# Optimization experiments

Hardware: AMD Instinct MI355X
Metric: run time of the kernel (lower is better)

## Reference

```python
import jax, jax.numpy as jnp
import numpy as np

N = 100000   # nodes
E = 1600000  # edges
F = 256      # feature_dim
H = 64       # hidden_dim == out_channels
HEADS = 1


def setup_inputs() -> dict:
    key = jax.random.key(0)
    ks = jax.random.split(key, 12)
    x = jax.random.normal(ks[0], (N, F), dtype=jnp.float32)
    edge_index = jax.random.randint(ks[1], (2, E), 0, N, dtype=jnp.int32)
    s = 0.05
    params = {
        'W_proj': jax.random.normal(ks[2], (F, H), dtype=jnp.float32) * s,
        'b_proj': jnp.zeros((H,), dtype=jnp.float32),
        'Wq1': jax.random.normal(ks[3], (H, HEADS * H), dtype=jnp.float32) * s,
        'Wk1': jax.random.normal(ks[4], (H, HEADS * H), dtype=jnp.float32) * s,
        'Wv1': jax.random.normal(ks[5], (H, HEADS * H), dtype=jnp.float32) * s,
        'Wq2': jax.random.normal(ks[6], (H, HEADS * H), dtype=jnp.float32) * s,
        'Wk2': jax.random.normal(ks[7], (H, HEADS * H), dtype=jnp.float32) * s,
        'Wv2': jax.random.normal(ks[8], (H, HEADS * H), dtype=jnp.float32) * s,
        'W_sig': jax.random.normal(ks[9], (H, 1), dtype=jnp.float32) * s,
        'b_sig': jnp.zeros((1,), dtype=jnp.float32),
    }
    return {'x': x, 'edge_index': edge_index, **params}


def _gat_layer(x, src, dst, Wq, Wk, Wv):
    # x: [N, H]; src/dst: [E] (edge_index[0]=source j, edge_index[1]=dest i)
    n = x.shape[0]
    q = (x @ Wq).reshape(n, HEADS, H)
    k = (x @ Wk).reshape(n, HEADS, H)
    v = (x @ Wv).reshape(n, HEADS, H)
    # edge-wise scores: (q_i * k_j).sum(-1) / sqrt(out_channels)
    scores = jnp.einsum('ehc,ehc->eh', q[dst], k[src]) / np.float32(np.sqrt(H))
    alpha = jax.nn.relu(scores)                                  # [E, HEADS]
    # segment softmax over destination neighborhoods (numerically stable)
    m = jax.ops.segment_max(alpha, dst, num_segments=n)          # [N, HEADS]
    m = jnp.where(jnp.isfinite(m), m, jnp.float32(0.0))
    e = jnp.exp(alpha - m[dst])
    denom = jax.ops.segment_sum(e, dst, num_segments=n)
    a = e / (denom[dst] + jnp.float32(1e-16))                    # [E, HEADS]
    # scatter-weighted sum of values to destinations
    out = jax.ops.segment_sum(v[src] * a[:, :, None], dst, num_segments=n)
    return out.mean(axis=1), a                                   # [N, H], [E, HEADS]


def reference(x, edge_index, W_proj, b_proj, Wq1, Wk1, Wv1, Wq2, Wk2, Wv2, W_sig, b_sig):
    src, dst = edge_index[0], edge_index[1]
    h = jax.nn.gelu(x @ W_proj + b_proj, approximate=False)
    h, attn1 = _gat_layer(h, src, dst, Wq1, Wk1, Wv1)
    h = jax.nn.gelu(h, approximate=False)
    h, attn2 = _gat_layer(h, src, dst, Wq2, Wk2, Wv2)
    signals = h @ W_sig + b_sig                                  # [N, 1]
    return signals, attn1, attn2
```

## Files before the change

kernel.cpp:

```cpp
#include <hip/hip_runtime.h>
#include <hip/hip_fp16.h>
#include <math.h>

#define FF 256
#define HH 64

typedef __attribute__((ext_vector_type(8))) short short8;
typedef __attribute__((ext_vector_type(4))) float f32x4;

__device__ __forceinline__ float gelu_f(float x) {
    float ax = fabsf(x) * 0.70710678118654752f;
    float t = __builtin_amdgcn_rcpf(fmaf(0.3275911f, ax, 1.0f));
    float poly = t * fmaf(t, fmaf(t, fmaf(t, fmaf(t, 1.061405429f, -1.453152027f),
                  1.421413741f), -0.284496736f), 0.254829592f);
    float er = 1.0f - poly * __expf(-ax * ax);
    er = (x < 0.f) ? -er : er;
    return 0.5f * x * (1.0f + er);
}

__device__ __forceinline__ unsigned short bf16rne(float f) {
    unsigned u = __float_as_uint(f);
    unsigned r = u + 0x7FFFu + ((u >> 16) & 1u);
    return (unsigned short)(r >> 16);
}

__device__ __forceinline__ void bf16split(float f, short& hi, short& lo) {
    unsigned u = __float_as_uint(f);
    unsigned r = u + 0x7FFFu + ((u >> 16) & 1u);
    hi = (short)(r >> 16);
    float fh = __uint_as_float(r & 0xFFFF0000u);
    float fl = f - fh;
    unsigned u2 = __float_as_uint(fl);
    unsigned r2 = u2 + 0x7FFFu + ((u2 >> 16) & 1u);
    lo = (short)(r2 >> 16);
}

__device__ __forceinline__ __half2 shfl_xor_h2(__half2 v, int off) {
    union { __half2 h; int i; } u;
    u.h = v;
    u.i = __shfl_xor(u.i, off, 64);
    return u.h;
}

__global__ __launch_bounds__(256) void k_wprep(
        const float* __restrict__ Wp,
        const float* __restrict__ Wq1, const float* __restrict__ Wk1, const float* __restrict__ Wv1,
        const float* __restrict__ Wq2, const float* __restrict__ Wk2, const float* __restrict__ Wv2,
        short* __restrict__ wf) {
    int total = 16384 + 6 * 4096;
    for (int gid = blockIdx.x * 256 + threadIdx.x; gid < total; gid += gridDim.x * 256) {
        const float* W;
        int fid, hibase, lobase;
        if (gid < 16384) {
            W = Wp; fid = gid; hibase = 0; lobase = 16384;
        } else {
            int t = gid - 16384;
            int m = t >> 12;
            fid = t & 4095;
            switch (m) {
                case 0: W = Wq1; break;
                case 1: W = Wk1; break;
                case 2: W = Wv1; break;
                case 3: W = Wq2; break;
                case 4: W = Wk2; break;
                default: W = Wv2; break;
            }
            hibase = 32768 + m * 8192;
            lobase = hibase + 4096;
        }
        int j    = fid & 7;
        int lane = (fid >> 3) & 63;
        int ct   = (fid >> 9) & 3;
        int s    = fid >> 11;
        int k    = s * 32 + (lane >> 4) * 8 + j;
        int col  = ct * 16 + (lane & 15);
        short hi, lo;
        bf16split(W[k * HH + col], hi, lo);
        wf[hibase + fid] = hi;
        wf[lobase + fid] = lo;
    }
}


__global__ __launch_bounds__(256) void k_partA(const int* __restrict__ dst,
        int* __restrict__ blockHist, int E, int PB, int NB) {
    __shared__ int hist[256];
    int t = threadIdx.x, bid = blockIdx.x;
    hist[t] = 0;
    __syncthreads();
    int base = bid * 4096;
    int e0 = base + t * 4;
    if (base + 4095 < E) {
        #pragma unroll
        for (int i = 0; i < 4; ++i) {
            int4 d = *reinterpret_cast<const int4*>(dst + e0 + i * 1024);
            atomicAdd(&hist[d.x >> 9], 1);
            atomicAdd(&hist[d.y >> 9], 1);
            atomicAdd(&hist[d.z >> 9], 1);
            atomicAdd(&hist[d.w >> 9], 1);
        }
    } else {
        for (int i = 0; i < 4; ++i)
            for (int j = 0; j < 4; ++j) {
                int e = e0 + i * 1024 + j;
                if (e < E) atomicAdd(&hist[dst[e] >> 9], 1);
            }
    }
    __syncthreads();
    if (t < NB) blockHist[t * PB + bid] = hist[t];
}

__global__ __launch_bounds__(512) void k_partA2(int* __restrict__ blockHist,
        int* __restrict__ bucketTotal, int PB) {
    __shared__ int buf[512];
    int t = threadIdx.x, b = blockIdx.x;
    int orig = (t < PB) ? blockHist[b * PB + t] : 0;
    buf[t] = orig;
    __syncthreads();
    #pragma unroll
    for (int off = 1; off < 512; off <<= 1) {
        int v = (t >= off) ? buf[t - off] : 0;
        __syncthreads();
        buf[t] += v;
        __syncthreads();
    }
    if (t < PB) blockHist[b * PB + t] = buf[t] - orig;
    if (t == 511) bucketTotal[b] = buf[511];
}

__global__ __launch_bounds__(256) void k_partA2b(const int* __restrict__ bucketTotal,
        int* __restrict__ bucketBase, int* __restrict__ rowptr, int NB, int N, int E) {
    __shared__ int buf[256];
    int t = threadIdx.x;
    int orig = (t < NB) ? bucketTotal[t] : 0;
    buf[t] = orig;
    __syncthreads();
    #pragma unroll
    for (int off = 1; off < 256; off <<= 1) {
        int v = (t >= off) ? buf[t - off] : 0;
        __syncthreads();
        buf[t] += v;
        __syncthreads();
    }
    if (t < NB) bucketBase[t] = buf[t] - orig;
    if (t == 0) { bucketBase[NB] = buf[255]; rowptr[N] = E; }
}

__device__ __forceinline__ void do_partB(int bid, const int* __restrict__ src,
        const int* __restrict__ dst, const int* __restrict__ blockBase,
        const int* __restrict__ bucketBase,
        int* __restrict__ bps, int* __restrict__ beid, int E, int PB, int NB) {
    if (bid >= PB) return;
    __shared__ int hist[256], lstart[256], cur[256], basec[256];
    __shared__ int spack[4096], seid_[4096], gtar[4096];
    int t = threadIdx.x;
    hist[t] = 0;
    __syncthreads();
    int base = bid * 4096;
    int e0 = base + t * 4;
    bool full = (base + 4095 < E);
    if (full) {
        #pragma unroll
        for (int i = 0; i < 4; ++i) {
            int4 d = *reinterpret_cast<const int4*>(dst + e0 + i * 1024);
            atomicAdd(&hist[d.x >> 9], 1);
            atomicAdd(&hist[d.y >> 9], 1);
            atomicAdd(&hist[d.z >> 9], 1);
            atomicAdd(&hist[d.w >> 9], 1);
        }
    } else {
        for (int i = 0; i < 4; ++i)
            for (int j = 0; j < 4; ++j) {
                int e = e0 + i * 1024 + j;
                if (e < E) atomicAdd(&hist[dst[e] >> 9], 1);
            }
    }
    __syncthreads();
    int h0 = hist[t];
    lstart[t] = h0;
    __syncthreads();
    #pragma unroll
    for (int off = 1; off < 256; off <<= 1) {
        int v = (t >= off) ? lstart[t - off] : 0;
        __syncthreads();
        lstart[t] += v;
        __syncthreads();
    }
    int excl = lstart[t] - h0;
    __syncthreads();
    lstart[t] = excl;
    cur[t]    = excl;
    basec[t]  = (t < NB) ? (bucketBase[t] + blockBase[t * PB + bid] - excl) : 0;
    __syncthreads();
    auto place = [&](int d, int s, int e) {
        int bu = d >> 9;
        int pos = atomicAdd(&cur[bu], 1);
        spack[pos] = ((d & 511) << 17) | s;
        seid_[pos] = e;
        gtar[pos]  = basec[bu] + pos;
    };
    if (full) {
        #pragma unroll
        for (int i = 0; i < 4; ++i) {
            int4 d = *reinterpret_cast<const int4*>(dst + e0 + i * 1024);
            int4 s = *reinterpret_cast<const int4*>(src + e0 + i * 1024);
            int eb = e0 + i * 1024;
            place(d.x, s.x, eb);
            place(d.y, s.y, eb + 1);
            place(d.z, s.z, eb + 2);
            place(d.w, s.w, eb + 3);
        }
    } else {
        for (int i = 0; i < 4; ++i)
            for (int j = 0; j < 4; ++j) {
                int e = e0 + i * 1024 + j;
                if (e < E) place(dst[e], src[e], e);
            }
    }
    __syncthreads();
    int count = min(4096, E - base);
    #pragma unroll
    for (int i = 0; i < 16; ++i) {
        int sidx = t + i * 256;
        if (sidx < count) {
            int g = gtar[sidx];
            bps[g]  = spack[sidx];
            beid[g] = seid_[sidx];
        }
    }
}

__device__ __forceinline__ void do_partC(int b, const int* __restrict__ bps,
        const int* __restrict__ beid, const int* __restrict__ bucketBase,
        int* __restrict__ rowptr, int* __restrict__ esrc, int* __restrict__ inv,
        int N, int NB) {
    if (b >= NB) return;
    __shared__ int cnt[512], sc[512], cur[512], pairbuf[256];
    int t = threadIdx.x;
    cnt[t] = 0; cnt[t + 256] = 0;
    cur[t] = 0; cur[t + 256] = 0;
    __syncthreads();
    int rB = bucketBase[b], rE = bucketBase[b + 1];
    for (int p = rB + t; p < rE; p += 256)
        atomicAdd(&cnt[bps[p] >> 17], 1);
    __syncthreads();
    int a  = cnt[2 * t], b2 = cnt[2 * t + 1];
    int ps = a + b2;
    pairbuf[t] = ps;
    __syncthreads();
    #pragma unroll
    for (int off = 1; off < 256; off <<= 1) {
        int v = (t >= off) ? pairbuf[t - off] : 0;
        __syncthreads();
        pairbuf[t] += v;
        __syncthreads();
    }
    int pex = pairbuf[t] - ps;
    sc[2 * t]     = pex;
    sc[2 * t + 1] = pex + a;
    __syncthreads();
    int lo = b << 9;
    #pragma unroll
    for (int i = 0; i < 2; ++i) {
        int idx = t + i * 256;
        int node = lo + idx;
        if (node < N) rowptr[node] = rB + sc[idx];
    }
    for (int p = rB + t; p < rE; p += 256) {
        int u = bps[p];
        int local = u >> 17;
        int s = u & 0x1FFFF;
        int r = atomicAdd(&cur[local], 1);
        int pos = rB + sc[local] + r;
        esrc[pos] = s;
        inv[beid[p]] = pos;
    }
}

__device__ __forceinline__ void do_attn(int bid, const float* __restrict__ ecsr,
        const int* __restrict__ inv, float* __restrict__ attn, int E) {
    int e0 = (bid * 256 + threadIdx.x) * 4;
    if (e0 + 3 < E) {
        int4 i4 = *reinterpret_cast<const int4*>(inv + e0);
        float4 a;
        a.x = ecsr[i4.x]; a.y = ecsr[i4.y]; a.z = ecsr[i4.z]; a.w = ecsr[i4.w];
        *reinterpret_cast<float4*>(attn + e0) = a;
    } else {
        for (int e = e0; e < E; ++e) attn[e] = ecsr[inv[e]];
    }
}

__device__ __forceinline__ void do_proj(int bid, const float* __restrict__ x,
        const short* __restrict__ wf, const float* __restrict__ b,
        float* __restrict__ h, int n) {
    if (bid * 64 >= n) return;
    int lane = threadIdx.x & 63;
    int w    = threadIdx.x >> 6;
    int m    = lane & 15, g = lane >> 4;
    int rowc = min(bid * 64 + w * 16 + m, n - 1);
    const float* xrow = x + (size_t)rowc * FF + g * 8;
    const short* wlo = wf + 16384;
    f32x4 acc[4];
    #pragma unroll
    for (int ct = 0; ct < 4; ++ct) acc[ct] = (f32x4){0.f, 0.f, 0.f, 0.f};
    #pragma unroll
    for (int s = 0; s < 8; ++s) {
        float4 a0 = *reinterpret_cast<const float4*>(xrow + s * 32);
        float4 a1 = *reinterpret_cast<const float4*>(xrow + s * 32 + 4);
        float av[8] = {a0.x, a0.y, a0.z, a0.w, a1.x, a1.y, a1.z, a1.w};
        short8 ah, al;
        #pragma unroll
        for (int j = 0; j < 8; ++j) { short hi, lo; bf16split(av[j], hi, lo); ah[j] = hi; al[j] = lo; }
        #pragma unroll
        for (int ct = 0; ct < 4; ++ct) {
            int fo = ((s * 4 + ct) * 64 + lane) * 8;
            short8 bh = *reinterpret_cast<const short8*>(wf + fo);
            short8 bl = *reinterpret_cast<const short8*>(wlo + fo);
            acc[ct] = __builtin_amdgcn_mfma_f32_16x16x32_bf16(ah, bh, acc[ct], 0, 0, 0);
            acc[ct] = __builtin_amdgcn_mfma_f32_16x16x32_bf16(al, bh, acc[ct], 0, 0, 0);
            acc[ct] = __builtin_amdgcn_mfma_f32_16x16x32_bf16(ah, bl, acc[ct], 0, 0, 0);
        }
    }
    int orow0 = bid * 64 + w * 16 + g * 4;
    #pragma unroll
    for (int ct = 0; ct < 4; ++ct) {
        int col = ct * 16 + m;
        float bias = b[col];
        #pragma unroll
        for (int r = 0; r < 4; ++r) {
            int row = orow0 + r;
            if (row < n) h[(size_t)row * HH + col] = acc[ct][r] + bias;
        }
    }
}

__device__ __forceinline__ void do_qkv(int bid, const float* __restrict__ hsrc,
        const short* __restrict__ wfq, const short* __restrict__ wfk, const short* __restrict__ wfv,
        __half* __restrict__ qh, __half* __restrict__ kv, int n) {
    if (bid * 64 >= n) return;
    int lane = threadIdx.x & 63;
    int w    = threadIdx.x >> 6;
    int m    = lane & 15, g = lane >> 4;
    int rowc = min(bid * 64 + w * 16 + m, n - 1);
    const float* hrow = hsrc + (size_t)rowc * HH + g * 8;
    f32x4 aq[4], ak[4], av_[4];
    #pragma unroll
    for (int ct = 0; ct < 4; ++ct) {
        aq[ct] = (f32x4){0.f, 0.f, 0.f, 0.f};
        ak[ct] = (f32x4){0.f, 0.f, 0.f, 0.f};
        av_[ct] = (f32x4){0.f, 0.f, 0.f, 0.f};
    }
    #pragma unroll
    for (int s = 0; s < 2; ++s) {
        float4 a0 = *reinterpret_cast<const float4*>(hrow + s * 32);
        float4 a1 = *reinterpret_cast<const float4*>(hrow + s * 32 + 4);
        float avv[8] = {a0.x, a0.y, a0.z, a0.w, a1.x, a1.y, a1.z, a1.w};
        short8 ah;
        #pragma unroll
        for (int j = 0; j < 8; ++j) ah[j] = (short)bf16rne(gelu_f(avv[j]));
        #pragma unroll
        for (int ct = 0; ct < 4; ++ct) {
            int fo = ((s * 4 + ct) * 64 + lane) * 8;
            short8 qh8 = *reinterpret_cast<const short8*>(wfq + fo);
            short8 ql8 = *reinterpret_cast<const short8*>(wfq + 4096 + fo);
            short8 kh8 = *reinterpret_cast<const short8*>(wfk + fo);
            short8 kl8 = *reinterpret_cast<const short8*>(wfk + 4096 + fo);
            short8 vh8 = *reinterpret_cast<const short8*>(wfv + fo);
            short8 vl8 = *reinterpret_cast<const short8*>(wfv + 4096 + fo);
            aq[ct] = __builtin_amdgcn_mfma_f32_16x16x32_bf16(ah, qh8, aq[ct], 0, 0, 0);
            aq[ct] = __builtin_amdgcn_mfma_f32_16x16x32_bf16(ah, ql8, aq[ct], 0, 0, 0);
            ak[ct] = __builtin_amdgcn_mfma_f32_16x16x32_bf16(ah, kh8, ak[ct], 0, 0, 0);
            ak[ct] = __builtin_amdgcn_mfma_f32_16x16x32_bf16(ah, kl8, ak[ct], 0, 0, 0);
            av_[ct] = __builtin_amdgcn_mfma_f32_16x16x32_bf16(ah, vh8, av_[ct], 0, 0, 0);
            av_[ct] = __builtin_amdgcn_mfma_f32_16x16x32_bf16(ah, vl8, av_[ct], 0, 0, 0);
        }
    }
    int orow0 = bid * 64 + w * 16 + g * 4;
    #pragma unroll
    for (int ct = 0; ct < 4; ++ct) {
        int col = ct * 16 + m;
        int cb  = (col >> 3) * 16 + (col & 7);
        #pragma unroll
        for (int r = 0; r < 4; ++r) {
            int row = orow0 + r;
            if (row < n) {
                qh[(size_t)row * HH + col]     = __float2half(aq[ct][r]);
                kv[(size_t)row * 128 + cb]     = __float2half(ak[ct][r]);
                kv[(size_t)row * 128 + cb + 8] = __float2half(av_[ct][r]);
            }
        }
    }
}

__global__ __launch_bounds__(256) void k_proj_partB(
        const float* __restrict__ x, const short* __restrict__ wf,
        const float* __restrict__ b, float* __restrict__ h, int n,
        const int* __restrict__ src, const int* __restrict__ dst,
        const int* __restrict__ blockBase, const int* __restrict__ bucketBase,
        int* __restrict__ bps, int* __restrict__ beid, int E, int PB, int NB) {
    int bid = blockIdx.x >> 1;
    if ((blockIdx.x & 1) == 0) do_proj(bid, x, wf, b, h, n);
    else                       do_partB(bid, src, dst, blockBase, bucketBase, bps, beid, E, PB, NB);
}

__global__ __launch_bounds__(256) void k_qkv_partC(
        const float* __restrict__ hsrc,
        const short* __restrict__ wfq, const short* __restrict__ wfk, const short* __restrict__ wfv,
        __half* __restrict__ qh, __half* __restrict__ kv, int n,
        const int* __restrict__ bps, const int* __restrict__ beid,
        const int* __restrict__ bucketBase,
        int* __restrict__ rowptr, int* __restrict__ esrc, int* __restrict__ inv, int NB) {
    int bid = blockIdx.x >> 1;
    if ((blockIdx.x & 1) == 0) do_qkv(bid, hsrc, wfq, wfk, wfv, qh, kv, n);
    else                       do_partC(bid, bps, beid, bucketBase, rowptr, esrc, inv, n, NB);
}

__global__ __launch_bounds__(256) void k_qkv_attn(
        const float* __restrict__ hsrc,
        const short* __restrict__ wfq, const short* __restrict__ wfk, const short* __restrict__ wfv,
        __half* __restrict__ qh, __half* __restrict__ kv, int n,
        const float* __restrict__ ecsr, const int* __restrict__ inv,
        float* __restrict__ attn, int E) {
    int bid = blockIdx.x >> 1;
    if ((blockIdx.x & 1) == 0) do_qkv(bid, hsrc, wfq, wfk, wfv, qh, kv, n);
    else                       do_attn(bid, ecsr, inv, attn, E);
}

__global__ __launch_bounds__(256) void k_attn(const float* __restrict__ ecsr,
        const int* __restrict__ inv, float* __restrict__ attn, int E) {
    do_attn(blockIdx.x, ecsr, inv, attn, E);
}

template<bool LAST>
__global__ __launch_bounds__(256) void k_edge(
        const __half* __restrict__ qarr, const __half* __restrict__ kv,
        const int* __restrict__ rowptr,
        const int* __restrict__ esrc,
        float* __restrict__ ecsr,
        float* __restrict__ hout,
        float* __restrict__ signals,
        const float* __restrict__ Wsig, const float* __restrict__ bsig,
        int n) {
    int node = blockIdx.x * 4 + (threadIdx.x >> 6);
    if (node >= n) return;
    int lane = threadIdx.x & 63;
    int li = lane & 7, g = lane >> 3;
    int start = rowptr[node], end = rowptr[node + 1];
    int deg = end - start;
    __half2 q2[4];
    {
        union { uint4 u; __half2 h[4]; } Q;
        Q.u = *reinterpret_cast<const uint4*>(qarr + (size_t)node * HH + li * 8);
        #pragma unroll
        for (int j = 0; j < 4; ++j) q2[j] = Q.h[j];
    }
    int p0 = start + lane;
    int el = (p0 < end) ? esrc[p0] : 0;

    __half2 acc2[4];
    #pragma unroll
    for (int j = 0; j < 4; ++j) acc2[j] = __float2half2_rn(0.f);
    float s = 0.f;
    for (int c = 0; c < deg; c += 16) {
        int idx0 = c + g, idx1 = c + 8 + g;
        bool v0 = idx0 < deg, v1 = idx1 < deg;
        int sv0, sv1;
        if (c + 16 <= 64) {
            sv0 = __shfl(el, idx0);
            sv1 = __shfl(el, idx1);
        } else {
            sv0 = v0 ? esrc[start + idx0] : 0;
            sv1 = v1 ? esrc[start + idx1] : 0;
        }
        const __half* b0 = kv + (size_t)sv0 * 128 + li * 16;
        const __half* b1 = kv + (size_t)sv1 * 128 + li * 16;
        union { uint4 u; __half2 h[4]; } K0, V0, K1, V1;
        K0.u = *reinterpret_cast<const uint4*>(b0);
        V0.u = *reinterpret_cast<const uint4*>(b0 + 8);
        K1.u = *reinterpret_cast<const uint4*>(b1);
        V1.u = *reinterpret_cast<const uint4*>(b1 + 8);
        __half2 d20 = __float2half2_rn(0.f);
        __half2 d21 = __float2half2_rn(0.f);
        #pragma unroll
        for (int j = 0; j < 4; ++j) {
            d20 = __hfma2(q2[j], K0.h[j], d20);
            d21 = __hfma2(q2[j], K1.h[j], d21);
        }
        float d0 = __low2float(d20) + __high2float(d20);
        float d1 = __low2float(d21) + __high2float(d21);
        d0 += __shfl_xor(d0, 1); d1 += __shfl_xor(d1, 1);
        d0 += __shfl_xor(d0, 2); d1 += __shfl_xor(d1, 2);
        d0 += __shfl_xor(d0, 4); d1 += __shfl_xor(d1, 4);
        float e0 = v0 ? __expf(fmaxf(d0 * 0.125f, 0.f)) : 0.f;
        float e1 = v1 ? __expf(fmaxf(d1 * 0.125f, 0.f)) : 0.f;
        s += e0 + e1;
        if (v0 && li == 0) ecsr[start + idx0] = e0;
        if (v1 && li == 0) ecsr[start + idx1] = e1;
        __half2 e20 = __float2half2_rn(e0);
        __half2 e21 = __float2half2_rn(e1);
        #pragma unroll
        for (int j = 0; j < 4; ++j) {
            acc2[j] = __hfma2(e20, V0.h[j], acc2[j]);
            acc2[j] = __hfma2(e21, V1.h[j], acc2[j]);
        }
    }
    #pragma unroll
    for (int off = 8; off < 64; off <<= 1) {
        s += __shfl_xor(s, off);
        #pragma unroll
        for (int j = 0; j < 4; ++j)
            acc2[j] = __hadd2(acc2[j], shfl_xor_h2(acc2[j], off));
    }
    float inv = 1.0f / (s + 1e-16f);
    float af[8];
    #pragma unroll
    for (int j = 0; j < 4; ++j) {
        af[2 * j]     = __low2float(acc2[j]);
        af[2 * j + 1] = __high2float(acc2[j]);
    }

    if (!LAST) {
        if (g == 0) {
            float4 o0, o1;
            o0.x = af[0] * inv; o0.y = af[1] * inv; o0.z = af[2] * inv; o0.w = af[3] * inv;
            o1.x = af[4] * inv; o1.y = af[5] * inv; o1.z = af[6] * inv; o1.w = af[7] * inv;
            *reinterpret_cast<float4*>(hout + (size_t)node * HH + li * 8)     = o0;
            *reinterpret_cast<float4*>(hout + (size_t)node * HH + li * 8 + 4) = o1;
        }
    } else {
        float4 w0 = *reinterpret_cast<const float4*>(Wsig + li * 8);
        float4 w1 = *reinterpret_cast<const float4*>(Wsig + li * 8 + 4);
        float t = af[0] * w0.x + af[1] * w0.y + af[2] * w0.z + af[3] * w0.w
                + af[4] * w1.x + af[5] * w1.y + af[6] * w1.z + af[7] * w1.w;
        t *= inv;
        t += __shfl_xor(t, 1);
        t += __shfl_xor(t, 2);
        t += __shfl_xor(t, 4);
        if (lane == 0) signals[node] = t + bsig[0];
    }
    for (int p = p0; p < end; p += 64)
        ecsr[p] *= inv;
}

extern "C" void kernel_launch(void* const* d_in, const int* in_sizes, int n_in,
                              void* d_out, int out_size, void* d_ws, size_t ws_size,
                              hipStream_t stream) {
    const float* x   = (const float*)d_in[0];
    const int*   ei  = (const int*)  d_in[1];
    const float* Wp  = (const float*)d_in[2];
    const float* bp  = (const float*)d_in[3];
    const float* Wq1 = (const float*)d_in[4];
    const float* Wk1 = (const float*)d_in[5];
    const float* Wv1 = (const float*)d_in[6];
    const float* Wq2 = (const float*)d_in[7];
    const float* Wk2 = (const float*)d_in[8];
    const float* Wv2 = (const float*)d_in[9];
    const float* Wsg = (const float*)d_in[10];
    const float* bsg = (const float*)d_in[11];

    const int N = in_sizes[0] / FF;
    const int E = in_sizes[1] / 2;
    const int* src = ei;
    const int* dst = ei + E;

    const int NB = (N + 511) >> 9;
    const int PB = (E + 4095) >> 12;

    char* ws = (char*)d_ws;
    size_t off = 0;
    auto alloc = [&](size_t bytes) -> void* {
        void* p = ws + off;
        off += (bytes + 255) & ~(size_t)255;
        return p;
    };
    __half* qh   = (__half*)alloc((size_t)N * HH * 2);
    __half* kv   = (__half*)alloc((size_t)N * 128 * 2);
    float* h     = (float*)alloc((size_t)N * HH * 4);
    float* ecsr  = (float*)alloc((size_t)E * 4);
    int* inv     = (int*)alloc((size_t)E * 4);
    int* esrc    = (int*)alloc((size_t)E * 4);
    int* bps     = (int*)alloc((size_t)E * 4);
    int* beid    = (int*)alloc((size_t)E * 4);
    int* rowptr  = (int*)alloc((size_t)(N + 1) * 4);
    int* blockHist   = (int*)alloc((size_t)NB * PB * 4);
    int* bucketTotal = (int*)alloc((size_t)NB * 4);
    int* bucketBase  = (int*)alloc((size_t)(NB + 1) * 4);
    short* wf    = (short*)alloc((size_t)81920 * 2);

    float* out     = (float*)d_out;
    float* signals = out;
    float* attn1   = out + N;
    float* attn2   = out + N + E;

    k_wprep<<<64, 256, 0, stream>>>(Wp, Wq1, Wk1, Wv1, Wq2, Wk2, Wv2, wf);

    k_partA<<<PB, 256, 0, stream>>>(dst, blockHist, E, PB, NB);
    k_partA2<<<NB, 512, 0, stream>>>(blockHist, bucketTotal, PB);
    k_partA2b<<<1, 256, 0, stream>>>(bucketTotal, bucketBase, rowptr, NB, N, E);

    int gemmBlocks = (N + 63) / 64;
    int e4Blocks   = ((E + 3) / 4 + 255) / 256;
    int fusedB     = 2 * max(gemmBlocks, PB);
    int fusedC     = 2 * max(gemmBlocks, NB);
    int fusedA     = 2 * max(gemmBlocks, e4Blocks);

    k_proj_partB<<<fusedB, 256, 0, stream>>>(x, wf, bp, h, N,
            src, dst, blockHist, bucketBase, bps, beid, E, PB, NB);

    const short* wfbase = wf + 32768;
    k_qkv_partC<<<fusedC, 256, 0, stream>>>(h, wfbase, wfbase + 8192, wfbase + 16384,
            qh, kv, N, bps, beid, bucketBase, rowptr, esrc, inv, NB);
    k_edge<false><<<(N + 3) / 4, 256, 0, stream>>>(qh, kv, rowptr, esrc,
            ecsr, h, nullptr, nullptr, nullptr, N);

    k_qkv_attn<<<fusedA, 256, 0, stream>>>(h, wfbase + 24576, wfbase + 32768, wfbase + 40960,
            qh, kv, N, ecsr, inv, attn1, E);
    k_edge<true><<<(N + 3) / 4, 256, 0, stream>>>(qh, kv, rowptr, esrc,
            ecsr, nullptr, signals, Wsg, bsg, N);
    k_attn<<<e4Blocks, 256, 0, stream>>>(ecsr, inv, attn2, E);
}
```

Baseline: 313.8 us.

## Scatter packed 64-bit edge records directly and defer inverse-permutation writes

The bucket-partition pass now writes one 64-bit record per edge (local dst, src and edge id) straight to its global slot via shared-memory atomic cursors. This drops the per-block histogram, prefix scan and LDS staging. The CSR build pass writes a position array instead of the scattered inv writes, and those writes move into a new pass fused with the first edge-attention kernel. The aim is to shorten the serial partition phase and overlap the random inv scatter with edge compute, at the cost of uncoalesced 8-byte global scatters and more bytes moved.

Result: slower. 333.9 us (+6.4%).

```diff
diff --git a/kernel.cpp b/kernel.cpp
--- a/kernel.cpp
+++ b/kernel.cpp
@@ -7,6 +7,7 @@
 
 typedef __attribute__((ext_vector_type(8))) short short8;
 typedef __attribute__((ext_vector_type(4))) float f32x4;
+typedef unsigned long long ull;
 
 __device__ __forceinline__ float gelu_f(float x) {
     float ax = fabsf(x) * 0.70710678118654752f;
@@ -146,69 +147,32 @@
     if (t == 0) { bucketBase[NB] = buf[255]; rowptr[N] = E; }
 }
 
-__device__ __forceinline__ void do_partB(int bid, const int* __restrict__ src,
+__device__ __forceinline__ void do_partB3(int bid, const int* __restrict__ src,
         const int* __restrict__ dst, const int* __restrict__ blockBase,
         const int* __restrict__ bucketBase,
-        int* __restrict__ bps, int* __restrict__ beid, int E, int PB, int NB) {
+        ull* __restrict__ bps, int E, int PB, int NB) {
     if (bid >= PB) return;
-    __shared__ int hist[256], lstart[256], cur[256], basec[256];
-    __shared__ int spack[4096], seid_[4096], gtar[4096];
+    __shared__ int cur[256];
     int t = threadIdx.x;
-    hist[t] = 0;
+    if (t < NB) cur[t] = bucketBase[t] + blockBase[t * PB + bid];
     __syncthreads();
     int base = bid * 4096;
     int e0 = base + t * 4;
-    bool full = (base + 4095 < E);
-    if (full) {
-        #pragma unroll
-        for (int i = 0; i < 4; ++i) {
-            int4 d = *reinterpret_cast<const int4*>(dst + e0 + i * 1024);
-            atomicAdd(&hist[d.x >> 9], 1);
-            atomicAdd(&hist[d.y >> 9], 1);
-            atomicAdd(&hist[d.z >> 9], 1);
-            atomicAdd(&hist[d.w >> 9], 1);
-        }
-    } else {
-        for (int i = 0; i < 4; ++i)
-            for (int j = 0; j < 4; ++j) {
-                int e = e0 + i * 1024 + j;
-                if (e < E) atomicAdd(&hist[dst[e] >> 9], 1);
-            }
-    }
-    __syncthreads();
-    int h0 = hist[t];
-    lstart[t] = h0;
-    __syncthreads();
-    #pragma unroll
-    for (int off = 1; off < 256; off <<= 1) {
-        int v = (t >= off) ? lstart[t - off] : 0;
-        __syncthreads();
-        lstart[t] += v;
-        __syncthreads();
-    }
-    int excl = lstart[t] - h0;
-    __syncthreads();
-    lstart[t] = excl;
-    cur[t]    = excl;
-    basec[t]  = (t < NB) ? (bucketBase[t] + blockBase[t * PB + bid] - excl) : 0;
-    __syncthreads();
     auto place = [&](int d, int s, int e) {
         int bu = d >> 9;
         int pos = atomicAdd(&cur[bu], 1);
-        spack[pos] = ((d & 511) << 17) | s;
-        seid_[pos] = e;
-        gtar[pos]  = basec[bu] + pos;
+        bps[pos] = ((ull)(d & 511) << 38) | ((ull)s << 21) | (unsigned)e;
     };
-    if (full) {
+    if (base + 4095 < E) {
         #pragma unroll
         for (int i = 0; i < 4; ++i) {
-            int4 d = *reinterpret_cast<const int4*>(dst + e0 + i * 1024);
-            int4 s = *reinterpret_cast<const int4*>(src + e0 + i * 1024);
+            int4 d4 = *reinterpret_cast<const int4*>(dst + e0 + i * 1024);
+            int4 s4 = *reinterpret_cast<const int4*>(src + e0 + i * 1024);
             int eb = e0 + i * 1024;
-            place(d.x, s.x, eb);
-            place(d.y, s.y, eb + 1);
-            place(d.z, s.z, eb + 2);
-            place(d.w, s.w, eb + 3);
+            place(d4.x, s4.x, eb);
+            place(d4.y, s4.y, eb + 1);
+            place(d4.z, s4.z, eb + 2);
+            place(d4.w, s4.w, eb + 3);
         }
     } else {
         for (int i = 0; i < 4; ++i)
@@ -217,22 +181,11 @@
                 if (e < E) place(dst[e], src[e], e);
             }
     }
-    __syncthreads();
-    int count = min(4096, E - base);
-    #pragma unroll
-    for (int i = 0; i < 16; ++i) {
-        int sidx = t + i * 256;
-        if (sidx < count) {
-            int g = gtar[sidx];
-            bps[g]  = spack[sidx];
-            beid[g] = seid_[sidx];
-        }
-    }
-}
-
-__device__ __forceinline__ void do_partC(int b, const int* __restrict__ bps,
-        const int* __restrict__ beid, const int* __restrict__ bucketBase,
-        int* __restrict__ rowptr, int* __restrict__ esrc, int* __restrict__ inv,
+}
+
+__device__ __forceinline__ void do_partC1(int b, const ull* __restrict__ bps,
+        const int* __restrict__ bucketBase,
+        int* __restrict__ rowptr, int* __restrict__ esrc, int* __restrict__ posArr,
         int N, int NB) {
     if (b >= NB) return;
     __shared__ int cnt[512], sc[512], cur[512], pairbuf[256];
@@ -242,7 +195,7 @@
     __syncthreads();
     int rB = bucketBase[b], rE = bucketBase[b + 1];
     for (int p = rB + t; p < rE; p += 256)
-        atomicAdd(&cnt[bps[p] >> 17], 1);
+        atomicAdd(&cnt[(int)(bps[p] >> 38)], 1);
     __syncthreads();
     int a  = cnt[2 * t], b2 = cnt[2 * t + 1];
     int ps = a + b2;
@@ -267,13 +220,29 @@
         if (node < N) rowptr[node] = rB + sc[idx];
     }
     for (int p = rB + t; p < rE; p += 256) {
-        int u = bps[p];
-        int local = u >> 17;
-        int s = u & 0x1FFFF;
+        ull u = bps[p];
+        int local = (int)(u >> 38);
+        int s = (int)((u >> 21) & 0x1FFFF);
         int r = atomicAdd(&cur[local], 1);
         int pos = rB + sc[local] + r;
         esrc[pos] = s;
-        inv[beid[p]] = pos;
+        posArr[p] = pos;
+    }
+}
+
+__device__ __forceinline__ void do_partC2(int bid, const ull* __restrict__ bps,
+        const int* __restrict__ posArr, int* __restrict__ inv, int E) {
+    int p0 = (bid * 256 + threadIdx.x) * 4;
+    if (p0 + 3 < E) {
+        ull u0 = bps[p0], u1 = bps[p0 + 1], u2 = bps[p0 + 2], u3 = bps[p0 + 3];
+        int4 ps = *reinterpret_cast<const int4*>(posArr + p0);
+        inv[(int)(u0 & 0x1FFFFF)] = ps.x;
+        inv[(int)(u1 & 0x1FFFFF)] = ps.y;
+        inv[(int)(u2 & 0x1FFFFF)] = ps.z;
+        inv[(int)(u3 & 0x1FFFFF)] = ps.w;
+    } else {
+        for (int p = p0; p < E; ++p)
+            inv[(int)(bps[p] & 0x1FFFFF)] = posArr[p];
     }
 }
 
@@ -392,47 +361,8 @@
     }
 }
 
-__global__ __launch_bounds__(256) void k_proj_partB(
-        const float* __restrict__ x, const short* __restrict__ wf,
-        const float* __restrict__ b, float* __restrict__ h, int n,
-        const int* __restrict__ src, const int* __restrict__ dst,
-        const int* __restrict__ blockBase, const int* __restrict__ bucketBase,
-        int* __restrict__ bps, int* __restrict__ beid, int E, int PB, int NB) {
-    int bid = blockIdx.x >> 1;
-    if ((blockIdx.x & 1) == 0) do_proj(bid, x, wf, b, h, n);
-    else                       do_partB(bid, src, dst, blockBase, bucketBase, bps, beid, E, PB, NB);
-}
-
-__global__ __launch_bounds__(256) void k_qkv_partC(
-        const float* __restrict__ hsrc,
-        const short* __restrict__ wfq, const short* __restrict__ wfk, const short* __restrict__ wfv,
-        __half* __restrict__ qh, __half* __restrict__ kv, int n,
-        const int* __restrict__ bps, const int* __restrict__ beid,
-        const int* __restrict__ bucketBase,
-        int* __restrict__ rowptr, int* __restrict__ esrc, int* __restrict__ inv, int NB) {
-    int bid = blockIdx.x >> 1;
-    if ((blockIdx.x & 1) == 0) do_qkv(bid, hsrc, wfq, wfk, wfv, qh, kv, n);
-    else                       do_partC(bid, bps, beid, bucketBase, rowptr, esrc, inv, n, NB);
-}
-
-__global__ __launch_bounds__(256) void k_qkv_attn(
-        const float* __restrict__ hsrc,
-        const short* __restrict__ wfq, const short* __restrict__ wfk, const short* __restrict__ wfv,
-        __half* __restrict__ qh, __half* __restrict__ kv, int n,
-        const float* __restrict__ ecsr, const int* __restrict__ inv,
-        float* __restrict__ attn, int E) {
-    int bid = blockIdx.x >> 1;
-    if ((blockIdx.x & 1) == 0) do_qkv(bid, hsrc, wfq, wfk, wfv, qh, kv, n);
-    else                       do_attn(bid, ecsr, inv, attn, E);
-}
-
-__global__ __launch_bounds__(256) void k_attn(const float* __restrict__ ecsr,
-        const int* __restrict__ inv, float* __restrict__ attn, int E) {
-    do_attn(blockIdx.x, ecsr, inv, attn, E);
-}
-
 template<bool LAST>
-__global__ __launch_bounds__(256) void k_edge(
+__device__ __forceinline__ void do_edge(int ebid,
         const __half* __restrict__ qarr, const __half* __restrict__ kv,
         const int* __restrict__ rowptr,
         const int* __restrict__ esrc,
@@ -441,7 +371,7 @@
         float* __restrict__ signals,
         const float* __restrict__ Wsig, const float* __restrict__ bsig,
         int n) {
-    int node = blockIdx.x * 4 + (threadIdx.x >> 6);
+    int node = ebid * 4 + (threadIdx.x >> 6);
     if (node >= n) return;
     int lane = threadIdx.x & 63;
     int li = lane & 7, g = lane >> 3;
@@ -540,6 +470,65 @@
     }
     for (int p = p0; p < end; p += 64)
         ecsr[p] *= inv;
+}
+
+__global__ __launch_bounds__(256) void k_proj_partB3(
+        const float* __restrict__ x, const short* __restrict__ wf,
+        const float* __restrict__ b, float* __restrict__ h, int n,
+        const int* __restrict__ src, const int* __restrict__ dst,
+        const int* __restrict__ blockBase, const int* __restrict__ bucketBase,
+        ull* __restrict__ bps, int E, int PB, int NB) {
+    int bid = blockIdx.x >> 1;
+    if ((blockIdx.x & 1) == 0) do_proj(bid, x, wf, b, h, n);
+    else                       do_partB3(bid, src, dst, blockBase, bucketBase, bps, E, PB, NB);
+}
+
+__global__ __launch_bounds__(256) void k_qkv_partC1(
+        const float* __restrict__ hsrc,
+        const short* __restrict__ wfq, const short* __restrict__ wfk, const short* __restrict__ wfv,
+        __half* __restrict__ qh, __half* __restrict__ kv, int n,
+        const ull* __restrict__ bps, const int* __restrict__ bucketBase,
+        int* __restrict__ rowptr, int* __restrict__ esrc, int* __restrict__ posArr, int NB) {
+    int bid = blockIdx.x >> 1;
+    if ((blockIdx.x & 1) == 0) do_qkv(bid, hsrc, wfq, wfk, wfv, qh, kv, n);
+    else                       do_partC1(bid, bps, bucketBase, rowptr, esrc, posArr, n, NB);
+}
+
+__global__ __launch_bounds__(256) void k_edge1_partC2(
+        const __half* __restrict__ qarr, const __half* __restrict__ kv,
+        const int* __restrict__ rowptr, const int* __restrict__ esrc,
+        float* __restrict__ ecsr, float* __restrict__ hout, int n,
+        const ull* __restrict__ bps, const int* __restrict__ posArr,
+        int* __restrict__ inv, int E, int C2B) {
+    int bid = blockIdx.x >> 1;
+    if ((blockIdx.x & 1) == 0)
+        do_edge<false>(bid, qarr, kv, rowptr, esrc, ecsr, hout, nullptr, nullptr, nullptr, n);
+    else if (bid < C2B)
+        do_partC2(bid, bps, posArr, inv, E);
+}
+
+__global__ __launch_bounds__(256) void k_qkv_attn(
+        const float* __restrict__ hsrc,
+        const short* __restrict__ wfq, const short* __restrict__ wfk, const short* __restrict__ wfv,
+        __half* __restrict__ qh, __half* __restrict__ kv, int n,
+        const float* __restrict__ ecsr, const int* __restrict__ inv,
+        float* __restrict__ attn, int E) {
+    int bid = blockIdx.x >> 1;
+    if ((blockIdx.x & 1) == 0) do_qkv(bid, hsrc, wfq, wfk, wfv, qh, kv, n);
+    else                       do_attn(bid, ecsr, inv, attn, E);
+}
+
+__global__ __launch_bounds__(256) void k_edge2(
+        const __half* __restrict__ qarr, const __half* __restrict__ kv,
+        const int* __restrict__ rowptr, const int* __restrict__ esrc,
+        float* __restrict__ ecsr, float* __restrict__ signals,
+        const float* __restrict__ Wsig, const float* __restrict__ bsig, int n) {
+    do_edge<true>(blockIdx.x, qarr, kv, rowptr, esrc, ecsr, nullptr, signals, Wsig, bsig, n);
+}
+
+__global__ __launch_bounds__(256) void k_attn(const float* __restrict__ ecsr,
+        const int* __restrict__ inv, float* __restrict__ attn, int E) {
+    do_attn(blockIdx.x, ecsr, inv, attn, E);
 }
 
 extern "C" void kernel_launch(void* const* d_in, const int* in_sizes, int n_in,
@@ -579,8 +568,8 @@
     float* ecsr  = (float*)alloc((size_t)E * 4);
     int* inv     = (int*)alloc((size_t)E * 4);
     int* esrc    = (int*)alloc((size_t)E * 4);
-    int* bps     = (int*)alloc((size_t)E * 4);
-    int* beid    = (int*)alloc((size_t)E * 4);
+    int* posArr  = (int*)alloc((size_t)E * 4);
+    ull* bps     = (ull*)alloc((size_t)E * 8);
     int* rowptr  = (int*)alloc((size_t)(N + 1) * 4);
     int* blockHist   = (int*)alloc((size_t)NB * PB * 4);
     int* bucketTotal = (int*)alloc((size_t)NB * 4);
@@ -600,22 +589,26 @@
 
     int gemmBlocks = (N + 63) / 64;
     int e4Blocks   = ((E + 3) / 4 + 255) / 256;
-    int fusedB     = 2 * max(gemmBlocks, PB);
-    int fusedC     = 2 * max(gemmBlocks, NB);
-    int fusedA     = 2 * max(gemmBlocks, e4Blocks);
-
-    k_proj_partB<<<fusedB, 256, 0, stream>>>(x, wf, bp, h, N,
-            src, dst, blockHist, bucketBase, bps, beid, E, PB, NB);
+    int edgeBlocks = (N + 3) / 4;
+
+    int f1 = 2 * max(gemmBlocks, PB);
+    k_proj_partB3<<<f1, 256, 0, stream>>>(x, wf, bp, h, N,
+            src, dst, blockHist, bucketBase, bps, E, PB, NB);
 
     const short* wfbase = wf + 32768;
-    k_qkv_partC<<<fusedC, 256, 0, stream>>>(h, wfbase, wfbase + 8192, wfbase + 16384,
-            qh, kv, N, bps, beid, bucketBase, rowptr, esrc, inv, NB);
-    k_edge<false><<<(N + 3) / 4, 256, 0, stream>>>(qh, kv, rowptr, esrc,
-            ecsr, h, nullptr, nullptr, nullptr, N);
-
-    k_qkv_attn<<<fusedA, 256, 0, stream>>>(h, wfbase + 24576, wfbase + 32768, wfbase + 40960,
+    int f2 = 2 * max(gemmBlocks, NB);
+    k_qkv_partC1<<<f2, 256, 0, stream>>>(h, wfbase, wfbase + 8192, wfbase + 16384,
+            qh, kv, N, bps, bucketBase, rowptr, esrc, posArr, NB);
+
+    int f3 = 2 * max(edgeBlocks, e4Blocks);
+    k_edge1_partC2<<<f3, 256, 0, stream>>>(qh, kv, rowptr, esrc, ecsr, h, N,
+            bps, posArr, inv, E, e4Blocks);
+
+    int f4 = 2 * max(gemmBlocks, e4Blocks);
+    k_qkv_attn<<<f4, 256, 0, stream>>>(h, wfbase + 24576, wfbase + 32768, wfbase + 40960,
             qh, kv, N, ecsr, inv, attn1, E);
-    k_edge<true><<<(N + 3) / 4, 256, 0, stream>>>(qh, kv, rowptr, esrc,
-            ecsr, nullptr, signals, Wsg, bsg, N);
+
+    k_edge2<<<edgeBlocks, 256, 0, stream>>>(qh, kv, rowptr, esrc, ecsr,
+            signals, Wsg, bsg, N);
     k_attn<<<e4Blocks, 256, 0, stream>>>(ecsr, inv, attn2, E);
 }
```
